# Optimization experiments

Hardware: AMD Instinct MI355X
Metric: run time of the kernel (lower is better)

## Reference

```python
import jax, jax.numpy as jnp
import numpy as np

B, T, I, H = 64, 512, 256, 256


def setup_inputs() -> dict:
    key = jax.random.key(0)
    ks = jax.random.split(key, 5)
    s = 1.0 / np.sqrt(H)
    return {
        "x": jax.random.normal(ks[0], (B, T, I), dtype=jnp.float32),
        "W_ih": jax.random.uniform(ks[1], (4 * H, I), jnp.float32, -s, s),
        "W_hh": jax.random.uniform(ks[2], (4 * H, H), jnp.float32, -s, s),
        "b_ih": jax.random.uniform(ks[3], (4 * H,), jnp.float32, -s, s),
        "b_hh": jax.random.uniform(ks[4], (4 * H,), jnp.float32, -s, s),
    }


def reference(x, W_ih, W_hh, b_ih, b_hh):
    # PyTorch LSTM gate order: input, forget, cell(g), output.
    # Precompute input projection for all timesteps: [B, T, 4H]
    x_proj = jnp.einsum("bti,gi->btg", x, W_ih) + b_ih + b_hh

    def step(carry, xt):
        h, c = carry                       # [B, H] each
        gates = xt + h @ W_hh.T            # [B, 4H]
        i, f, g, o = jnp.split(gates, 4, axis=-1)
        i = jax.nn.sigmoid(i)
        f = jax.nn.sigmoid(f)
        g = jnp.tanh(g)
        o = jax.nn.sigmoid(o)
        c = f * c + i * g
        h = o * jnp.tanh(c)
        return (h, c), h

    h0 = jnp.zeros((x.shape[0], W_hh.shape[1]), x.dtype)
    c0 = jnp.zeros_like(h0)
    (hT, cT), ys = jax.lax.scan(step, (h0, c0), jnp.swapaxes(x_proj, 0, 1))
    y = jnp.swapaxes(ys, 0, 1)             # [B, T, H], batch_first
    # Matches torch: (output, (h_n, c_n)) with num_layers*num_dirs = 1
    return y, hT[None], cT[None]
```

## Files before the change

### kernel.cpp

```cpp
#include <hip/hip_runtime.h>
#include <hip/hip_bf16.h>
#include <stdint.h>

#define Bz 64
#define Tz 512
#define Iz 256
#define Hz 256
#define G4z 1024
#define YSZ (Bz*Tz*Hz)

typedef __bf16 bf16;
typedef float  f32x4  __attribute__((ext_vector_type(4)));
typedef int    i32x4  __attribute__((ext_vector_type(4)));
typedef __bf16 bf16x8 __attribute__((ext_vector_type(8)));
typedef __bf16 bf16x4 __attribute__((ext_vector_type(4)));

#define XP_OFF  0u
#define XB_OFF  67108864u
#define WI_OFF  83886080u

__global__ __launch_bounds__(256) void cvt_f32_bf16(const float* __restrict__ in,
                                                    bf16* __restrict__ out, int n4) {
  int i = blockIdx.x * blockDim.x + threadIdx.x;
  if (i >= n4) return;
  float4 v = reinterpret_cast<const float4*>(in)[i];
  bf16x4 o = {(__bf16)v.x, (__bf16)v.y, (__bf16)v.z, (__bf16)v.w};
  *reinterpret_cast<bf16x4*>(out + (size_t)i*4) = o;
}

__global__ __launch_bounds__(256) void xproj_gemm(const bf16* __restrict__ A,
                                                  const bf16* __restrict__ Bw,
                                                  const float* __restrict__ b_ih,
                                                  const float* __restrict__ b_hh,
                                                  bf16* __restrict__ xp) {
  constexpr int K = 256;
  __shared__ __align__(16) bf16 As[128*32];
  __shared__ __align__(16) bf16 Bs[128*32];
  __shared__ float bias_s[128];
  const int bm = blockIdx.x >> 3;
  const int bn = blockIdx.x & 7;
  const int m0 = bm * 128, n0 = bn * 128;
  const int tid = threadIdx.x;
  if (tid < 128) bias_s[tid] = b_ih[n0 + tid] + b_hh[n0 + tid];
  const int w = tid >> 6, lane = tid & 63;
  const int wm = w >> 1, wn = w & 1;
  const int lr = lane & 15, lk = lane >> 4;
  f32x4 acc[4][4] = {};
  for (int kt = 0; kt < 8; ++kt) {
#pragma unroll
    for (int p = 0; p < 2; ++p) {
      int elem = p * 256 + tid;
      int row = elem >> 2, c = elem & 3;
      uint4 va = *reinterpret_cast<const uint4*>(A + (size_t)(m0 + row) * K + kt*32 + c*8);
      *reinterpret_cast<uint4*>((char*)As + row*64 + ((c ^ (row & 3)) * 16)) = va;
      uint4 vb = *reinterpret_cast<const uint4*>(Bw + (size_t)(n0 + row) * K + kt*32 + c*8);
      *reinterpret_cast<uint4*>((char*)Bs + row*64 + ((c ^ (row & 3)) * 16)) = vb;
    }
    __syncthreads();
    bf16x8 fa[4], fb[4];
#pragma unroll
    for (int f = 0; f < 4; ++f) {
      int ra = wm*64 + f*16 + lr;
      fa[f] = *reinterpret_cast<const bf16x8*>((char*)As + ra*64 + ((lk ^ (ra & 3)) * 16));
      int rb = wn*64 + f*16 + lr;
      fb[f] = *reinterpret_cast<const bf16x8*>((char*)Bs + rb*64 + ((lk ^ (rb & 3)) * 16));
    }
#pragma unroll
    for (int fi = 0; fi < 4; ++fi)
#pragma unroll
      for (int fj = 0; fj < 4; ++fj)
        acc[fi][fj] = __builtin_amdgcn_mfma_f32_16x16x32_bf16(fa[fi], fb[fj], acc[fi][fj], 0, 0, 0);
    __syncthreads();
  }
#pragma unroll
  for (int fi = 0; fi < 4; ++fi)
#pragma unroll
    for (int fj = 0; fj < 4; ++fj) {
      int col = n0 + wn*64 + fj*16 + lr;
      float bias = bias_s[wn*64 + fj*16 + lr];
#pragma unroll
      for (int v = 0; v < 4; ++v) {
        int row = m0 + wm*64 + fi*16 + lk*4 + v;
        xp[(size_t)row * 1024 + col] = (__bf16)(acc[fi][fj][v] + bias);
      }
    }
}


__device__ __forceinline__ float fast_sigmoid(float x) {
  return __builtin_amdgcn_rcpf(1.f + __expf(-x));
}
__device__ __forceinline__ float fast_tanh(float x) {
  return 1.f - 2.f * __builtin_amdgcn_rcpf(__expf(2.f * x) + 1.f);
}
__device__ __forceinline__ int sdot4f(int a, int b, int c) {
#if __has_builtin(__builtin_amdgcn_sdot4)
  return __builtin_amdgcn_sdot4(a, b, c, false);
#else
  int r = c;
  r += (int)(signed char)(a)        * (int)(signed char)(b);
  r += (int)(signed char)(a >> 8)   * (int)(signed char)(b >> 8);
  r += (int)(signed char)(a >> 16)  * (int)(signed char)(b >> 16);
  r += (int)(signed char)(a >> 24)  * (int)(signed char)(b >> 24);
  return r;
#endif
}
#define SCL (1.0f / (2032.0f * 127.0f))

__global__ __launch_bounds__(512, 2) void lstm_rec(const bf16* __restrict__ xp,
                                                   const float* __restrict__ Whh,
                                                   float* __restrict__ out) {
  __shared__ __align__(16) char h_s[2][256];
  const int tid = threadIdx.x;
  const int b = blockIdx.x;
  const int h = tid >> 1;
  const int sel = tid & 1;
  const int r0 = sel * 256 + h;
  const int r1 = r0 + 512;

  int w0[64], w1[64];
  {
    const float* wp0 = Whh + (size_t)r0 * 256;
    const float* wp1 = Whh + (size_t)r1 * 256;
#pragma unroll
    for (int d = 0; d < 64; ++d) {
      float4 f = *reinterpret_cast<const float4*>(wp0 + d*4);
      int q0 = (int)rintf(f.x * 2032.f), q1 = (int)rintf(f.y * 2032.f);
      int q2 = (int)rintf(f.z * 2032.f), q3 = (int)rintf(f.w * 2032.f);
      w0[d] = (q0 & 255) | ((q1 & 255) << 8) | ((q2 & 255) << 16) | ((q3 & 255) << 24);
      float4 g = *reinterpret_cast<const float4*>(wp1 + d*4);
      int p0 = (int)rintf(g.x * 2032.f), p1 = (int)rintf(g.y * 2032.f);
      int p2 = (int)rintf(g.z * 2032.f), p3 = (int)rintf(g.w * 2032.f);
      w1[d] = (p0 & 255) | ((p1 & 255) << 8) | ((p2 & 255) << 16) | ((p3 & 255) << 24);
    }
  }
  if (tid < 64) reinterpret_cast<int*>(h_s[0])[tid] = 0;

  const bf16* xprow = xp + (size_t)b * Tz * 1024;
  unsigned short xv0 = *(const unsigned short*)(xprow + r0);
  unsigned short xv1 = *(const unsigned short*)(xprow + r1);

  float cc = 0.f;
  __syncthreads();

  for (int t = 0; t < Tz; ++t) {
    const char* hb = h_s[t & 1];
    int a0=0,a1=0,a2=0,a3=0, d0=0,d1=0,d2=0,d3=0;
#pragma unroll
    for (int d = 0; d < 16; ++d) {
      i32x4 hv = *reinterpret_cast<const i32x4*>(hb + d*16);
      a0 = sdot4f(hv[0], w0[4*d+0], a0);
      a1 = sdot4f(hv[1], w0[4*d+1], a1);
      a2 = sdot4f(hv[2], w0[4*d+2], a2);
      a3 = sdot4f(hv[3], w0[4*d+3], a3);
      d0 = sdot4f(hv[0], w1[4*d+0], d0);
      d1 = sdot4f(hv[1], w1[4*d+1], d1);
      d2 = sdot4f(hv[2], w1[4*d+2], d2);
      d3 = sdot4f(hv[3], w1[4*d+3], d3);
    }
    float g0 = (float)((a0 + a1) + (a2 + a3)) * SCL + __uint_as_float((unsigned)xv0 << 16);
    float g1 = (float)((d0 + d1) + (d2 + d3)) * SCL + __uint_as_float((unsigned)xv1 << 16);
    if (t < Tz - 1) {
      xv0 = *(const unsigned short*)(xprow + (size_t)(t+1)*1024 + r0);
      xv1 = *(const unsigned short*)(xprow + (size_t)(t+1)*1024 + r1);
    }
    float p0 = __shfl_xor(g0, 1);
    float p1 = __shfl_xor(g1, 1);
    float vi = sel ? p0 : g0;
    float vf = sel ? g0 : p0;
    float vg = sel ? p1 : g1;
    float vo = sel ? g1 : p1;
    float gi = fast_sigmoid(vi);
    float gf = fast_sigmoid(vf);
    float gg = fast_tanh(vg);
    float go = fast_sigmoid(vo);
    cc = gf * cc + gi * gg;
    float hv = go * fast_tanh(cc);
    if (!sel) {
      out[((size_t)b * Tz + t) * 256 + h] = hv;
      if (t < Tz - 1) {
        h_s[(t & 1) ^ 1][h] = (char)(int)rintf(hv * 127.f);
      } else {
        out[(size_t)YSZ + (size_t)b * 256 + h] = hv;
        out[(size_t)YSZ + 16384 + (size_t)b * 256 + h] = cc;
      }
    }
    __syncthreads();
  }
}

extern "C" void kernel_launch(void* const* d_in, const int* in_sizes, int n_in,
                              void* d_out, int out_size, void* d_ws, size_t ws_size,
                              hipStream_t stream) {
  const float* x    = (const float*)d_in[0];
  const float* W_ih = (const float*)d_in[1];
  const float* W_hh = (const float*)d_in[2];
  const float* b_ih = (const float*)d_in[3];
  const float* b_hh = (const float*)d_in[4];
  float* out = (float*)d_out;
  char* ws = (char*)d_ws;

  bf16* xp  = (bf16*)(ws + XP_OFF);
  bf16* xb  = (bf16*)(ws + XB_OFF);
  bf16* wib = (bf16*)(ws + WI_OFF);

  cvt_f32_bf16<<<8192, 256, 0, stream>>>(x, xb, (Bz*Tz*Iz) / 4);
  cvt_f32_bf16<<<256, 256, 0, stream>>>(W_ih, wib, (G4z*Iz) / 4);
  xproj_gemm<<<2048, 256, 0, stream>>>(xb, wib, b_ih, b_hh, xp);
  lstm_rec<<<64, 512, 0, stream>>>(xp, W_hh, out);
}
```

Measured before the change: 604.3 us.

## Cut LSTM step latency: prefetch xp two steps ahead, DPP swap, gate activation before exchange

In the recurrent kernel, each thread now applies its own gate nonlinearities before the pair exchange. Sigmoid or tanh is chosen per lane so that only two transcendentals are computed before swapping, instead of four after it. The lane swap uses a DPP quad-permute move in place of a shuffle, and xp is now prefetched two timesteps ahead rather than one to hide global-load latency. The per-step __syncthreads is replaced by an inline s_waitcnt lgkmcnt(0) plus s_barrier, which skips waiting on outstanding vector memory ops such as the prefetch loads and output stores. This risks correctness if the compiler relies on the barrier for memory ordering.

```diff
diff --git a/kernel.cpp b/kernel.cpp
--- a/kernel.cpp
+++ b/kernel.cpp
@@ -87,12 +87,6 @@
 }
 
 
-__device__ __forceinline__ float fast_sigmoid(float x) {
-  return __builtin_amdgcn_rcpf(1.f + __expf(-x));
-}
-__device__ __forceinline__ float fast_tanh(float x) {
-  return 1.f - 2.f * __builtin_amdgcn_rcpf(__expf(2.f * x) + 1.f);
-}
 __device__ __forceinline__ int sdot4f(int a, int b, int c) {
 #if __has_builtin(__builtin_amdgcn_sdot4)
   return __builtin_amdgcn_sdot4(a, b, c, false);
@@ -105,6 +99,13 @@
   return r;
 #endif
 }
+__device__ __forceinline__ float pair_xor1(float v) {
+#if __has_builtin(__builtin_amdgcn_mov_dpp)
+  return __int_as_float(__builtin_amdgcn_mov_dpp(__float_as_int(v), 0xB1, 0xf, 0xf, true));
+#else
+  return __shfl_xor(v, 1);
+#endif
+}
 #define SCL (1.0f / (2032.0f * 127.0f))
 
 __global__ __launch_bounds__(512, 2) void lstm_rec(const bf16* __restrict__ xp,
@@ -114,8 +115,8 @@
   const int tid = threadIdx.x;
   const int b = blockIdx.x;
   const int h = tid >> 1;
-  const int sel = tid & 1;
-  const int r0 = sel * 256 + h;
+  const int s = tid & 1;
+  const int r0 = s * 256 + h;
   const int r1 = r0 + 512;
 
   int w0[64], w1[64];
@@ -137,14 +138,21 @@
   if (tid < 64) reinterpret_cast<int*>(h_s[0])[tid] = 0;
 
   const bf16* xprow = xp + (size_t)b * Tz * 1024;
-  unsigned short xv0 = *(const unsigned short*)(xprow + r0);
-  unsigned short xv1 = *(const unsigned short*)(xprow + r1);
+  unsigned short c0 = *(const unsigned short*)(xprow + r0);
+  unsigned short c1 = *(const unsigned short*)(xprow + r1);
+  unsigned short n0 = *(const unsigned short*)(xprow + 1024 + r0);
+  unsigned short n1 = *(const unsigned short*)(xprow + 1024 + r1);
 
   float cc = 0.f;
   __syncthreads();
 
   for (int t = 0; t < Tz; ++t) {
     const char* hb = h_s[t & 1];
+    unsigned short f0 = 0, f1 = 0;
+    if (t + 2 < Tz) {
+      f0 = *(const unsigned short*)(xprow + (size_t)(t+2)*1024 + r0);
+      f1 = *(const unsigned short*)(xprow + (size_t)(t+2)*1024 + r1);
+    }
     int a0=0,a1=0,a2=0,a3=0, d0=0,d1=0,d2=0,d3=0;
 #pragma unroll
     for (int d = 0; d < 16; ++d) {
@@ -158,25 +166,24 @@
       d2 = sdot4f(hv[2], w1[4*d+2], d2);
       d3 = sdot4f(hv[3], w1[4*d+3], d3);
     }
-    float g0 = (float)((a0 + a1) + (a2 + a3)) * SCL + __uint_as_float((unsigned)xv0 << 16);
-    float g1 = (float)((d0 + d1) + (d2 + d3)) * SCL + __uint_as_float((unsigned)xv1 << 16);
-    if (t < Tz - 1) {
-      xv0 = *(const unsigned short*)(xprow + (size_t)(t+1)*1024 + r0);
-      xv1 = *(const unsigned short*)(xprow + (size_t)(t+1)*1024 + r1);
-    }
-    float p0 = __shfl_xor(g0, 1);
-    float p1 = __shfl_xor(g1, 1);
-    float vi = sel ? p0 : g0;
-    float vf = sel ? g0 : p0;
-    float vg = sel ? p1 : g1;
-    float vo = sel ? g1 : p1;
-    float gi = fast_sigmoid(vi);
-    float gf = fast_sigmoid(vf);
-    float gg = fast_tanh(vg);
-    float go = fast_sigmoid(vo);
+    float g0 = (float)((a0 + a1) + (a2 + a3)) * SCL + __uint_as_float((unsigned)c0 << 16);
+    float g1 = (float)((d0 + d1) + (d2 + d3)) * SCL + __uint_as_float((unsigned)c1 << 16);
+    float e0 = __expf(-g0);
+    float act0 = __builtin_amdgcn_rcpf(1.f + e0);
+    float in1 = s ? -g1 : 2.f * g1;
+    float e1 = __expf(in1);
+    float dr = __builtin_amdgcn_rcpf(1.f + e1);
+    float act1 = s ? dr : 1.f - 2.f * dr;
+    float x0 = pair_xor1(act0);
+    float x1 = pair_xor1(act1);
+    float gi = s ? x0 : act0;
+    float gf = s ? act0 : x0;
+    float gg = s ? x1 : act1;
+    float go = s ? act1 : x1;
     cc = gf * cc + gi * gg;
-    float hv = go * fast_tanh(cc);
-    if (!sel) {
+    float e2 = __expf(2.f * cc);
+    float hv = go * (1.f - 2.f * __builtin_amdgcn_rcpf(1.f + e2));
+    if (!s) {
       out[((size_t)b * Tz + t) * 256 + h] = hv;
       if (t < Tz - 1) {
         h_s[(t & 1) ^ 1][h] = (char)(int)rintf(hv * 127.f);
@@ -185,7 +192,9 @@
         out[(size_t)YSZ + 16384 + (size_t)b * 256 + h] = cc;
       }
     }
-    __syncthreads();
+    if (t == Tz - 1) break;
+    c0 = n0; c1 = n1; n0 = f0; n1 = f1;
+    asm volatile("s_waitcnt lgkmcnt(0)\n\ts_barrier" ::: "memory");
   }
 }
 
```

Result: no change. 598.4 us (-1.0%).
